# Kernel tuning notes

Measured on AMD Instinct MI355X. Metric: run time of the kernel, lower is better.

Reference implementation:

```python
import jax, jax.numpy as jnp
import numpy as np

K = 20  # neighbors

def _edgeconv(x, W, b):
    # x: [B, C, N]; W: [O, 2C]; b: [O]
    xt = jnp.swapaxes(x, 1, 2)                      # [B, N, C]
    # pairwise (negative squared) distance: -|xi|^2 - 2 xi.xj ... wait torch: -xx - inner - xx^T
    inner = -2.0 * jnp.einsum('bic,bjc->bij', xt, xt)   # [B, N, N]
    xx = jnp.sum(xt * xt, axis=-1)                       # [B, N]
    pd = -xx[:, None, :] - inner - xx[:, :, None]        # [B, N, N]
    _, idx = jax.lax.top_k(pd, K)                        # [B, N, K] nearest neighbors
    # gather neighbor features: feat[b,n,k,:] = xt[b, idx[b,n,k], :]
    feat = jnp.take_along_axis(xt[:, None, :, :],        # [B,1,N,C]
                               idx[:, :, :, None], axis=2)  # [B, N, K, C]
    center = xt[:, :, None, :]                           # [B, N, 1, C]
    edge = jnp.concatenate([feat - center,
                            jnp.broadcast_to(center, feat.shape)], axis=-1)  # [B,N,K,2C]
    # 1x1 conv == linear over channel dim, then LeakyReLU(0.2)
    h = jnp.einsum('bnkc,oc->bnko', edge, W) + b         # [B, N, K, O]
    h = jnp.where(h >= 0, h, 0.2 * h)
    out = jnp.max(h, axis=2)                             # [B, N, O] (max over neighbors)
    return jnp.swapaxes(out, 1, 2)                       # [B, O, N]

def setup_inputs() -> dict:
    key = jax.random.key(0)
    k1, k2, k3 = jax.random.split(key, 3)
    B, C, N, O = 8, 64, 4096, 128
    x = jax.random.normal(k1, (B, C, N), dtype=jnp.float32)
    W = jax.random.normal(k2, (O, 2 * C), dtype=jnp.float32) * (1.0 / np.sqrt(2 * C))
    b = jax.random.normal(k3, (O,), dtype=jnp.float32) * 0.01
    return {"x": x, "W": W, "b": b}

def reference(x, W, b):
    return _edgeconv(x, W, b)
```

## Files before the change

### kernel.cpp

```cpp
#include <hip/hip_runtime.h>

#define BB 8
#define CC 64
#define OO 128
#define NN 4096
#define KNN 20
#define NT 256
#define NG 64
#define NCH 4
#define RING 9
#define TRIG 5
#define SPLITW 192
#define WSPL 384
#define TILEB (16 * SPLITW * 2)

typedef short bf16x8 __attribute__((ext_vector_type(8)));
typedef float f32x4 __attribute__((ext_vector_type(4)));
typedef const __attribute__((address_space(1))) unsigned int* gas_ptr;
typedef __attribute__((address_space(3))) unsigned int* las_ptr;

#define REP20(F, P) F(P,0) F(P,1) F(P,2) F(P,3) F(P,4) F(P,5) F(P,6) F(P,7) \
    F(P,8) F(P,9) F(P,10) F(P,11) F(P,12) F(P,13) F(P,14) F(P,15) F(P,16)   \
    F(P,17) F(P,18) F(P,19)

#define TS_DECL(P,k) float P##m##k = 1e30f; int P##p##k = -1;
#define TS_REPL(P,k)                                                        \
  { const bool _h = (P##kpos == (k));                                       \
    P##m##k = _h ? _d : P##m##k;                                            \
    P##p##k = _h ? _j : P##p##k; }

#define TS_N(vd, xd, va, xa, vb, xb)                                        \
  { const bool _g = (vb) > (va); vd = _g ? (vb) : (va); xd = _g ? (xb) : (xa); }

#define TS_TREE(P)                                                          \
  { float t0,t1,t2,t3,t4,t5,t6,t7,t8,t9; int y0,y1,y2,y3,y4,y5,y6,y7,y8,y9; \
    TS_N(t0,y0, P##m0,0,  P##m1,1)   TS_N(t1,y1, P##m2,2,  P##m3,3)         \
    TS_N(t2,y2, P##m4,4,  P##m5,5)   TS_N(t3,y3, P##m6,6,  P##m7,7)         \
    TS_N(t4,y4, P##m8,8,  P##m9,9)   TS_N(t5,y5, P##m10,10, P##m11,11)      \
    TS_N(t6,y6, P##m12,12, P##m13,13) TS_N(t7,y7, P##m14,14, P##m15,15)     \
    TS_N(t8,y8, P##m16,16, P##m17,17) TS_N(t9,y9, P##m18,18, P##m19,19)     \
    float u0,u1,u2,u3,u4; int z0,z1,z2,z3,z4;                               \
    TS_N(u0,z0, t0,y0, t1,y1) TS_N(u1,z1, t2,y2, t3,y3)                     \
    TS_N(u2,z2, t4,y4, t5,y5) TS_N(u3,z3, t6,y6, t7,y7)                     \
    TS_N(u4,z4, t8,y8, t9,y9)                                               \
    float w0,w1; int q0,q1;                                                 \
    TS_N(w0,q0, u0,z0, u1,z1) TS_N(w1,q1, u2,z2, u3,z3)                     \
    float e0; int r0;                                                       \
    TS_N(e0,r0, w0,q0, w1,q1)                                               \
    TS_N(P##kmax, P##kpos, e0,r0, u4,z4) }

#define TS_INS(P, dval, jval)                                               \
  { const float _d = (dval); const int _j = (jval);                         \
    REP20(TS_REPL, P)                                                       \
    TS_TREE(P) }

#define RT_UPDATE                                                           \
  { const int _s1 = __builtin_amdgcn_ds_swizzle(__float_as_int(A_kmax), 0x101F); \
    const float _m1 = fminf(A_kmax, __int_as_float(_s1));                   \
    const int _s2 = __builtin_amdgcn_ds_swizzle(__float_as_int(_m1), 0x201F); \
    rt = fminf(_m1, __int_as_float(_s2)); }

__device__ __forceinline__ unsigned rne_bf16(float f) {
  const unsigned u = __float_as_uint(f);
  return (u + 0x7fffu + ((u >> 16) & 1u)) >> 16;
}

__global__ __launch_bounds__(128) void wsplit_kernel(
    const float* __restrict__ W, unsigned short* __restrict__ Wsp) {
  const int o = blockIdx.x;
  const int t = threadIdx.x;
  const float w = W[(size_t)o * (2 * CC) + t];
  const unsigned h = rne_bf16(w);
  const float r = w - __uint_as_float(h << 16);
  const unsigned m = rne_bf16(r);
  const float s = r - __uint_as_float(m << 16);
  const unsigned l = rne_bf16(s);
  unsigned short* row = Wsp + (size_t)o * WSPL;
  row[t] = (unsigned short)h;
  row[128 + t] = (unsigned short)m;
  row[256 + t] = (unsigned short)l;
}

__global__ __launch_bounds__(128, 3) void xprep_kernel(
    const float* __restrict__ x, float* __restrict__ xsq,
    unsigned short* __restrict__ xsp) {
  const int b = blockIdx.y;
  const int n = blockIdx.x * 128 + threadIdx.x;
  const float* xb = x + (size_t)b * CC * NN;

  float xr[CC];
  float sq = 0.f;
#pragma unroll
  for (int c = 0; c < CC; ++c) {
    xr[c] = xb[(size_t)c * NN + n];
    sq = fmaf(xr[c], xr[c], sq);
  }
  xsq[(size_t)b * NN + n] = sq;

  unsigned* srow = (unsigned*)(xsp + ((size_t)b * NN + n) * SPLITW);
#pragma unroll
  for (int c = 0; c < CC; c += 2) {
    const unsigned h0 = rne_bf16(xr[c]), h1 = rne_bf16(xr[c + 1]);
    const float r0 = xr[c] - __uint_as_float(h0 << 16);
    const float r1 = xr[c + 1] - __uint_as_float(h1 << 16);
    const unsigned m0 = rne_bf16(r0), m1 = rne_bf16(r1);
    const float s0 = r0 - __uint_as_float(m0 << 16);
    const float s1 = r1 - __uint_as_float(m1 << 16);
    const unsigned l0 = rne_bf16(s0), l1 = rne_bf16(s1);
    srow[c / 2] = h0 | (h1 << 16);
    srow[32 + c / 2] = m0 | (m1 << 16);
    srow[64 + c / 2] = l0 | (l1 << 16);
  }
}

#define MFMA6(ACC, B0, B1, B2, B3, B4, B5)                                  \
  f32x4 ACC;                                                                \
  { f32x4 a0 = {0.f,0.f,0.f,0.f}; f32x4 a1 = {0.f,0.f,0.f,0.f};             \
    f32x4 a2 = {0.f,0.f,0.f,0.f}; f32x4 a3 = {0.f,0.f,0.f,0.f};             \
    a0 = __builtin_amdgcn_mfma_f32_16x16x32_bf16(Ah0, B0, a0, 0, 0, 0);     \
    a1 = __builtin_amdgcn_mfma_f32_16x16x32_bf16(Ah1, B1, a1, 0, 0, 0);     \
    a2 = __builtin_amdgcn_mfma_f32_16x16x32_bf16(Ah0, B2, a2, 0, 0, 0);     \
    a3 = __builtin_amdgcn_mfma_f32_16x16x32_bf16(Ah1, B3, a3, 0, 0, 0);     \
    a0 = __builtin_amdgcn_mfma_f32_16x16x32_bf16(Am0, B0, a0, 0, 0, 0);     \
    a1 = __builtin_amdgcn_mfma_f32_16x16x32_bf16(Am1, B1, a1, 0, 0, 0);     \
    a2 = __builtin_amdgcn_mfma_f32_16x16x32_bf16(Ah0, B4, a2, 0, 0, 0);     \
    a3 = __builtin_amdgcn_mfma_f32_16x16x32_bf16(Ah1, B5, a3, 0, 0, 0);     \
    a0 = __builtin_amdgcn_mfma_f32_16x16x32_bf16(Al0, B0, a0, 0, 0, 0);     \
    a1 = __builtin_amdgcn_mfma_f32_16x16x32_bf16(Al1, B1, a1, 0, 0, 0);     \
    a2 = __builtin_amdgcn_mfma_f32_16x16x32_bf16(Am0, B2, a2, 0, 0, 0);     \
    a3 = __builtin_amdgcn_mfma_f32_16x16x32_bf16(Am1, B3, a3, 0, 0, 0);     \
    ACC = (a0 + a1) + (a2 + a3); }

__global__ __launch_bounds__(256, 3) void aq_kernel(
    const unsigned short* __restrict__ xsp,
    const unsigned short* __restrict__ Wsp, const float* __restrict__ bias,
    unsigned short* __restrict__ Ab16, float* __restrict__ Q) {
  const int b = blockIdx.y;
  const int wv = threadIdx.x >> 6;
  const int lane = threadIdx.x & 63;
  const int q = lane >> 4;
  const int c = lane & 15;
  const int nb = blockIdx.x * 64 + wv * 16;

  const unsigned short* arow =
      xsp + ((size_t)b * NN + nb + c) * SPLITW + q * 8;
  const bf16x8 Ah0 = *(const bf16x8*)(arow);
  const bf16x8 Ah1 = *(const bf16x8*)(arow + 32);
  const bf16x8 Am0 = *(const bf16x8*)(arow + 64);
  const bf16x8 Am1 = *(const bf16x8*)(arow + 96);
  const bf16x8 Al0 = *(const bf16x8*)(arow + 128);
  const bf16x8 Al1 = *(const bf16x8*)(arow + 160);

  unsigned short* Ab = Ab16 + (size_t)b * NN * OO;
  float* Qb = Q + (size_t)b * NN * OO;

#pragma unroll 2
  for (int ot = 0; ot < 8; ++ot) {
    const unsigned short* wrow = Wsp + (size_t)(ot * 16 + c) * WSPL + q * 8;
    const bf16x8 Ph0 = *(const bf16x8*)(wrow);
    const bf16x8 Ph1 = *(const bf16x8*)(wrow + 32);
    const bf16x8 Pm0 = *(const bf16x8*)(wrow + 128);
    const bf16x8 Pm1 = *(const bf16x8*)(wrow + 160);
    const bf16x8 Pl0 = *(const bf16x8*)(wrow + 256);
    const bf16x8 Pl1 = *(const bf16x8*)(wrow + 288);
    MFMA6(accP, Ph0, Ph1, Pm0, Pm1, Pl0, Pl1)
    const bf16x8 Gh0 = *(const bf16x8*)(wrow + 64);
    const bf16x8 Gh1 = *(const bf16x8*)(wrow + 96);
    const bf16x8 Gm0 = *(const bf16x8*)(wrow + 192);
    const bf16x8 Gm1 = *(const bf16x8*)(wrow + 224);
    const bf16x8 Gl0 = *(const bf16x8*)(wrow + 320);
    const bf16x8 Gl1 = *(const bf16x8*)(wrow + 352);
    MFMA6(accG, Gh0, Gh1, Gm0, Gm1, Gl0, Gl1)

    const float bv = bias[ot * 16 + c];
#pragma unroll
    for (int i = 0; i < 4; ++i) {
      const size_t row = (size_t)(nb + q * 4 + i);
      const float p = accP[i];
      Ab[row * OO + ot * 16 + c] = (unsigned short)rne_bf16(p);
      Qb[row * OO + ot * 16 + c] = accG[i] - p + bv;
    }
  }
}

#define STAGEG(G, BUF)                                                      \
  { const char* tb = (const char*)xspB + (size_t)(4 * (G) + wv) * TILEB + gof; \
    char* lb = (char*)(BUF) + wv * 6144;                                    \
    __builtin_amdgcn_global_load_lds((gas_ptr)(const void*)(tb), (las_ptr)(void*)(lb), 16, 0, 0); \
    __builtin_amdgcn_global_load_lds((gas_ptr)(const void*)(tb + 64), (las_ptr)(void*)(lb + 1024), 16, 0, 0); \
    __builtin_amdgcn_global_load_lds((gas_ptr)(const void*)(tb + 128), (las_ptr)(void*)(lb + 2048), 16, 0, 0); \
    __builtin_amdgcn_global_load_lds((gas_ptr)(const void*)(tb + 192), (las_ptr)(void*)(lb + 3072), 16, 0, 0); \
    __builtin_amdgcn_global_load_lds((gas_ptr)(const void*)(tb + 256), (las_ptr)(void*)(lb + 4096), 16, 0, 0); \
    __builtin_amdgcn_global_load_lds((gas_ptr)(const void*)(tb + 320), (las_ptr)(void*)(lb + 5120), 16, 0, 0); }

#define TILE_MFMA_L(LBUF, BUF)                                              \
  { const char* bb = (const char*)(LBUF) + c16;                             \
    const bf16x8 Bh0 = *(const bf16x8*)(bb + (q + 0) * 256);                \
    const bf16x8 Bh1 = *(const bf16x8*)(bb + (q + 4) * 256);                \
    const bf16x8 Bm0 = *(const bf16x8*)(bb + (q + 8) * 256);                \
    const bf16x8 Bm1 = *(const bf16x8*)(bb + (q + 12) * 256);               \
    const bf16x8 Bl0 = *(const bf16x8*)(bb + (q + 16) * 256);               \
    const bf16x8 Bl1 = *(const bf16x8*)(bb + (q + 20) * 256);               \
    f32x4 ac0 = {0.f, 0.f, 0.f, 0.f};                                       \
    f32x4 ac1 = {0.f, 0.f, 0.f, 0.f};                                       \
    f32x4 ac2 = {0.f, 0.f, 0.f, 0.f};                                       \
    f32x4 ac3 = {0.f, 0.f, 0.f, 0.f};                                       \
    ac0 = __builtin_amdgcn_mfma_f32_16x16x32_bf16(Ah0, Bh0, ac0, 0, 0, 0);  \
    ac1 = __builtin_amdgcn_mfma_f32_16x16x32_bf16(Ah1, Bh1, ac1, 0, 0, 0);  \
    ac2 = __builtin_amdgcn_mfma_f32_16x16x32_bf16(Ah0, Bm0, ac2, 0, 0, 0);  \
    ac3 = __builtin_amdgcn_mfma_f32_16x16x32_bf16(Ah1, Bm1, ac3, 0, 0, 0);  \
    ac0 = __builtin_amdgcn_mfma_f32_16x16x32_bf16(Am0, Bh0, ac0, 0, 0, 0);  \
    ac1 = __builtin_amdgcn_mfma_f32_16x16x32_bf16(Am1, Bh1, ac1, 0, 0, 0);  \
    ac2 = __builtin_amdgcn_mfma_f32_16x16x32_bf16(Ah0, Bl0, ac2, 0, 0, 0);  \
    ac3 = __builtin_amdgcn_mfma_f32_16x16x32_bf16(Ah1, Bl1, ac3, 0, 0, 0);  \
    ac0 = __builtin_amdgcn_mfma_f32_16x16x32_bf16(Al0, Bh0, ac0, 0, 0, 0);  \
    ac1 = __builtin_amdgcn_mfma_f32_16x16x32_bf16(Al1, Bh1, ac1, 0, 0, 0);  \
    ac2 = __builtin_amdgcn_mfma_f32_16x16x32_bf16(Am0, Bm0, ac2, 0, 0, 0);  \
    ac3 = __builtin_amdgcn_mfma_f32_16x16x32_bf16(Am1, Bm1, ac3, 0, 0, 0);  \
    const f32x4 acc = (ac0 + ac1) + (ac2 + ac3);                            \
    float* bw = &bounce[BUF][wv][0];                                        \
    bw[(q * 4 + 0) * 20 + c] = acc[0];                                      \
    bw[(q * 4 + 1) * 20 + c] = acc[1];                                      \
    bw[(q * 4 + 2) * 20 + c] = acc[2];                                      \
    bw[(q * 4 + 3) * 20 + c] = acc[3]; }

#define TILE_VALS(T, BUF)                                                   \
  const float* br = &bounce[BUF][wv][myrow * 20 + 4 * g];                   \
  const f32x4 dots = *(const f32x4*)br;                                     \
  const float4 xx = *(const float4*)(xsqb + (T) * 16 + 4 * g);              \
  const float d0 = fmaf(-2.f, dots[0], xx.x);                               \
  const float d1 = fmaf(-2.f, dots[1], xx.y);                               \
  const float d2 = fmaf(-2.f, dots[2], xx.z);                               \
  const float d3 = fmaf(-2.f, dots[3], xx.w);                               \
  const int jb = (T) * 16 + 4 * g;

#define TILE_SELF(T, BUF, K0, K1, K2, K3)                                   \
  { TILE_VALS(T, BUF)                                                       \
    A_m##K0 = d0; A_p##K0 = jb;                                             \
    A_m##K1 = d1; A_p##K1 = jb + 1;                                         \
    A_m##K2 = d2; A_p##K2 = jb + 2;                                         \
    A_m##K3 = d3; A_p##K3 = jb + 3; }

#define TILE_SEL(T, BUF)                                                    \
  { TILE_VALS(T, BUF)                                                       \
    if (d0 <= rt) { myring[cnt] = make_float2(d0, __int_as_float(jb)); ++cnt; } \
    if (d1 <= rt) { myring[cnt] = make_float2(d1, __int_as_float(jb + 1)); ++cnt; } \
    if (d2 <= rt) { myring[cnt] = make_float2(d2, __int_as_float(jb + 2)); ++cnt; } \
    if (d3 <= rt) { myring[cnt] = make_float2(d3, __int_as_float(jb + 3)); ++cnt; } \
    if (__ballot(cnt >= TRIG)) {                                            \
      for (int _k = 0; _k < cnt; ++_k) {                                    \
        const float2 e = myring[_k];                                        \
        if (e.x < A_kmax) { TS_INS(A_, e.x, __float_as_int(e.y)) }          \
      }                                                                     \
      cnt = 0;                                                              \
    }                                                                       \
    RT_UPDATE }

__global__ __launch_bounds__(256, 2) void knn_kernel(
    const unsigned short* __restrict__ xsp, const float* __restrict__ xsq,
    float* __restrict__ cd, int* __restrict__ ci) {
  __shared__ unsigned short Bbuf0[4 * TILEB / 2];
  __shared__ unsigned short Bbuf1[4 * TILEB / 2];
  __shared__ float bounce[2][4][16 * 20];
  __shared__ float2 ring[256][RING];

  const int b = blockIdx.y;
  const int wv = threadIdx.x >> 6;
  const int lane = threadIdx.x & 63;
  const int q = lane >> 4;
  const int c = lane & 15;
  const int c16 = c * 16;
  const int gof = c * 384 + q * 16;
  const int ibase = blockIdx.x * 64 + wv * 16;
  const int myrow = q * 4 + (c & 3);
  const int g = c >> 2;
  const int isel = ibase + myrow;

  const unsigned short* xspB = xsp + (size_t)b * NN * SPLITW;
  const float* xsqb = xsq + (size_t)b * NN;

  const unsigned short* arow = xspB + (size_t)(ibase + c) * SPLITW + q * 8;
  const bf16x8 Ah0 = *(const bf16x8*)(arow);
  const bf16x8 Ah1 = *(const bf16x8*)(arow + 32);
  const bf16x8 Am0 = *(const bf16x8*)(arow + 64);
  const bf16x8 Am1 = *(const bf16x8*)(arow + 96);
  const bf16x8 Al0 = *(const bf16x8*)(arow + 128);
  const bf16x8 Al1 = *(const bf16x8*)(arow + 160);

  REP20(TS_DECL, A_)
  float A_kmax = 1e30f; int A_kpos = 0;
  float rt = 1e30f;
  float2* myring = ring[threadIdx.x];
  int cnt = 0;

  STAGEG(0, Bbuf0)
  __syncthreads();
  STAGEG(1, Bbuf1)
  TILE_MFMA_L(Bbuf0 + 0 * 3072, 0)
  TILE_MFMA_L(Bbuf0 + 1 * 3072, 1) TILE_SELF(0, 0, 0, 1, 2, 3)
  TILE_MFMA_L(Bbuf0 + 2 * 3072, 0) TILE_SELF(1, 1, 4, 5, 6, 7)
  TILE_MFMA_L(Bbuf0 + 3 * 3072, 1) TILE_SELF(2, 0, 8, 9, 10, 11)
  __syncthreads();
  STAGEG(2, Bbuf0)
  TILE_MFMA_L(Bbuf1 + 0 * 3072, 0) TILE_SELF(3, 1, 12, 13, 14, 15)
  TILE_MFMA_L(Bbuf1 + 1 * 3072, 1) TILE_SELF(4, 0, 16, 17, 18, 19)
  TS_TREE(A_)
  RT_UPDATE
  TILE_MFMA_L(Bbuf1 + 2 * 3072, 0) TILE_SEL(5, 1)
  TILE_MFMA_L(Bbuf1 + 3 * 3072, 1) TILE_SEL(6, 0)
  __syncthreads();

  for (int G = 2; G < NG - 1; ++G) {
    unsigned short* cur = (G & 1) ? Bbuf1 : Bbuf0;
    unsigned short* nxt = (G & 1) ? Bbuf0 : Bbuf1;
    STAGEG(G + 1, nxt)
    const int t0 = 4 * G;
    TILE_MFMA_L(cur + 0 * 3072, 0) TILE_SEL(t0 - 1, 1)
    TILE_MFMA_L(cur + 1 * 3072, 1) TILE_SEL(t0, 0)
    TILE_MFMA_L(cur + 2 * 3072, 0) TILE_SEL(t0 + 1, 1)
    TILE_MFMA_L(cur + 3 * 3072, 1) TILE_SEL(t0 + 2, 0)
    __syncthreads();
  }

  TILE_MFMA_L(Bbuf1 + 0 * 3072, 0) TILE_SEL(251, 1)
  TILE_MFMA_L(Bbuf1 + 1 * 3072, 1) TILE_SEL(252, 0)
  TILE_MFMA_L(Bbuf1 + 2 * 3072, 0) TILE_SEL(253, 1)
  TILE_MFMA_L(Bbuf1 + 3 * 3072, 1) TILE_SEL(254, 0)
  TILE_SEL(255, 1)

  for (int _k = 0; _k < cnt; ++_k) {
    const float2 e = myring[_k];
    if (e.x < A_kmax) { TS_INS(A_, e.x, __float_as_int(e.y)) }
  }

  const size_t base = ((size_t)(b * NCH + g) * KNN) * NN + isel;
#define TS_ST(P,k) cd[base + (size_t)(k) * NN] = P##m##k; \
                   ci[base + (size_t)(k) * NN] = P##p##k;
  REP20(TS_ST, A_)
#undef TS_ST
}

#define TK_LIST(OP) OP(0) OP(1) OP(2) OP(3) OP(4) OP(5) OP(6) OP(7) OP(8) \
    OP(9) OP(10) OP(11) OP(12) OP(13) OP(14) OP(15) OP(16) OP(17) OP(18) OP(19)
#define TK_DECL(k) float td##k = 1e30f; int ti##k = -1;
#define TK_SW(a, b)                                                        \
  {                                                                        \
    const bool _s = (td##b < td##a) ||                                     \
                    ((td##b == td##a) && (ti##b < ti##a));                 \
    const float _fa = _s ? td##b : td##a;                                  \
    const float _fb = _s ? td##a : td##b;                                  \
    const int _ia = _s ? ti##b : ti##a;                                    \
    const int _ib = _s ? ti##a : ti##b;                                    \
    td##a = _fa; td##b = _fb; ti##a = _ia; ti##b = _ib;                    \
  }
#define TK_BUBBLE                                                          \
  TK_SW(18, 19) TK_SW(17, 18) TK_SW(16, 17) TK_SW(15, 16) TK_SW(14, 15)    \
  TK_SW(13, 14) TK_SW(12, 13) TK_SW(11, 12) TK_SW(10, 11) TK_SW(9, 10)     \
  TK_SW(8, 9) TK_SW(7, 8) TK_SW(6, 7) TK_SW(5, 6) TK_SW(4, 5)              \
  TK_SW(3, 4) TK_SW(2, 3) TK_SW(1, 2) TK_SW(0, 1)

__global__ __launch_bounds__(128, 4) void merge_kernel(
    const float* __restrict__ cd, const int* __restrict__ ci,
    int* __restrict__ idxf) {
  const int b = blockIdx.y;
  const int n = blockIdx.x * 128 + threadIdx.x;

  TK_LIST(TK_DECL)

  for (int ch = 0; ch < NCH; ++ch) {
    const size_t base = ((size_t)(b * NCH + ch) * KNN) * NN + n;
    for (int s = 0; s < KNN; ++s) {
      const float d = cd[base + (size_t)s * NN];
      const int j = ci[base + (size_t)s * NN];
      if ((d < td19) || ((d == td19) && (j < ti19))) {
        td19 = d;
        ti19 = j;
        TK_BUBBLE
      }
    }
  }

#define TK_STI(k) idxf[((size_t)b * KNN + (k)) * NN + n] = ti##k;
  TK_LIST(TK_STI)
#undef TK_STI
}

__global__ __launch_bounds__(256) void gather_kernel(
    const unsigned short* __restrict__ Ab16, const float* __restrict__ Q,
    const int* __restrict__ idxf, float* __restrict__ out) {
  __shared__ int jidx[KNN][32];
  __shared__ float ob[32][OO + 2];

  const int b = blockIdx.y;
  const int n0 = blockIdx.x * 32;
  const int t = threadIdx.x;
  const int p = t & 63;
  const int h = t >> 6;

  for (int e = t; e < KNN * 32; e += 256) {
    const int k = e >> 5, ii = e & 31;
    jidx[k][ii] = idxf[((size_t)b * KNN + k) * NN + n0 + ii];
  }
  __syncthreads();

  const unsigned short* Ab = Ab16 + (size_t)b * NN * OO;
  const float* Qb = Q + (size_t)b * NN * OO;

  for (int ii = h * 8; ii < h * 8 + 8; ++ii) {
    float m0 = -1e30f, m1 = -1e30f;
#pragma unroll
    for (int k = 0; k < KNN; ++k) {
      const unsigned v =
          *(const unsigned*)(Ab + (size_t)jidx[k][ii] * OO + 2 * p);
      m0 = fmaxf(m0, __uint_as_float(v << 16));
      m1 = fmaxf(m1, __uint_as_float(v & 0xFFFF0000u));
    }
    const float2 qv = *(const float2*)(Qb + (size_t)(n0 + ii) * OO + 2 * p);
    const float h0 = m0 + qv.x;
    const float h1 = m1 + qv.y;
    ob[ii][2 * p] = (h0 >= 0.f) ? h0 : 0.2f * h0;
    ob[ii][2 * p + 1] = (h1 >= 0.f) ? h1 : 0.2f * h1;
  }
  __syncthreads();

  float* ou = out + (size_t)b * OO * NN;
  for (int e = t; e < 32 * OO; e += 256) {
    const int ii = e & 31, oo = e >> 5;
    ou[(size_t)oo * NN + n0 + ii] = ob[ii][oo];
  }
}

extern "C" void kernel_launch(void* const* d_in, const int* in_sizes, int n_in,
                              void* d_out, int out_size, void* d_ws,
                              size_t ws_size, hipStream_t stream) {
  (void)in_sizes;
  (void)n_in;
  (void)out_size;
  (void)ws_size;
  const float* x = (const float*)d_in[0];
  const float* W = (const float*)d_in[1];
  const float* bias = (const float*)d_in[2];
  float* out = (float*)d_out;

  char* ws = (char*)d_ws;
  size_t off = 0;
  unsigned short* Ab16 = (unsigned short*)(ws + off);
  off += (size_t)BB * NN * OO * 2;
  float* Q = (float*)(ws + off);
  off += (size_t)BB * NN * OO * 4;
  float* xsq = (float*)(ws + off);
  off += (size_t)BB * NN * 4;
  unsigned short* xsp = (unsigned short*)(ws + off);
  off += (size_t)BB * NN * SPLITW * 2;
  float* cd = (float*)(ws + off);
  off += (size_t)BB * NCH * KNN * NN * 4;
  int* ci = (int*)(ws + off);
  off += (size_t)BB * NCH * KNN * NN * 4;
  int* idxf = (int*)(ws + off);
  off += (size_t)BB * KNN * NN * 4;
  unsigned short* Wsp = (unsigned short*)(ws + off);
  off += (size_t)OO * WSPL * 2;

  wsplit_kernel<<<dim3(OO), 128, 0, stream>>>(W, Wsp);
  xprep_kernel<<<dim3(NN / 128, BB), 128, 0, stream>>>(x, xsq, xsp);
  knn_kernel<<<dim3(NN / 64, BB), 256, 0, stream>>>(xsp, xsq, cd, ci);
  aq_kernel<<<dim3(NN / 64, BB), 256, 0, stream>>>(xsp, Wsp, bias, Ab16, Q);
  merge_kernel<<<dim3(NN / 128, BB), 128, 0, stream>>>(cd, ci, idxf);
  gather_kernel<<<dim3(NN / 32, BB), 256, 0, stream>>>(Ab16, Q, idxf, out);
}
```

Before: 534.0 us.

## Fuse top-k merge into knn kernel via cross-lane shuffles

The separate merge kernel is removed. Each knn thread now merges the four partial top-20 lists held by lanes in different column groups, using wave shuffles at lane offsets 4, 8 and 12 plus an insertion bubble sort, and lanes with g==0 write the final indices. This drops the global write and read of the candidate distance and index buffers and one kernel launch. In exchange the knn kernel's epilogue gets longer and needs more registers, which could lower occupancy or cause spills. Lanes with g!=0 also do redundant merge work whose shuffle sources may read out-of-range lanes, and those results are simply discarded.

```diff
diff --git a/kernel.cpp b/kernel.cpp
--- a/kernel.cpp
+++ b/kernel.cpp
@@ -7,7 +7,6 @@
 #define KNN 20
 #define NT 256
 #define NG 64
-#define NCH 4
 #define RING 9
 #define TRIG 5
 #define SPLITW 192
@@ -59,6 +58,25 @@
     const float _m1 = fminf(A_kmax, __int_as_float(_s1));                   \
     const int _s2 = __builtin_amdgcn_ds_swizzle(__float_as_int(_m1), 0x201F); \
     rt = fminf(_m1, __int_as_float(_s2)); }
+
+#define TK_LIST(OP) OP(0) OP(1) OP(2) OP(3) OP(4) OP(5) OP(6) OP(7) OP(8) \
+    OP(9) OP(10) OP(11) OP(12) OP(13) OP(14) OP(15) OP(16) OP(17) OP(18) OP(19)
+#define TK_DECL(k) float td##k = 1e30f; int ti##k = -1;
+#define TK_SW(a, b)                                                        \
+  {                                                                        \
+    const bool _s = (td##b < td##a) ||                                     \
+                    ((td##b == td##a) && (ti##b < ti##a));                 \
+    const float _fa = _s ? td##b : td##a;                                  \
+    const float _fb = _s ? td##a : td##b;                                  \
+    const int _ia = _s ? ti##b : ti##a;                                    \
+    const int _ib = _s ? ti##a : ti##b;                                    \
+    td##a = _fa; td##b = _fb; ti##a = _ia; ti##b = _ib;                    \
+  }
+#define TK_BUBBLE                                                          \
+  TK_SW(18, 19) TK_SW(17, 18) TK_SW(16, 17) TK_SW(15, 16) TK_SW(14, 15)    \
+  TK_SW(13, 14) TK_SW(12, 13) TK_SW(11, 12) TK_SW(10, 11) TK_SW(9, 10)     \
+  TK_SW(8, 9) TK_SW(7, 8) TK_SW(6, 7) TK_SW(5, 6) TK_SW(4, 5)              \
+  TK_SW(3, 4) TK_SW(2, 3) TK_SW(1, 2) TK_SW(0, 1)
 
 __device__ __forceinline__ unsigned rne_bf16(float f) {
   const unsigned u = __float_as_uint(f);
@@ -258,7 +276,7 @@
 
 __global__ __launch_bounds__(256, 2) void knn_kernel(
     const unsigned short* __restrict__ xsp, const float* __restrict__ xsq,
-    float* __restrict__ cd, int* __restrict__ ci) {
+    int* __restrict__ idxf) {
   __shared__ unsigned short Bbuf0[4 * TILEB / 2];
   __shared__ unsigned short Bbuf1[4 * TILEB / 2];
   __shared__ float bounce[2][4][16 * 20];
@@ -333,56 +351,30 @@
     if (e.x < A_kmax) { TS_INS(A_, e.x, __float_as_int(e.y)) }
   }
 
-  const size_t base = ((size_t)(b * NCH + g) * KNN) * NN + isel;
-#define TS_ST(P,k) cd[base + (size_t)(k) * NN] = P##m##k; \
-                   ci[base + (size_t)(k) * NN] = P##p##k;
-  REP20(TS_ST, A_)
-#undef TS_ST
-}
-
-#define TK_LIST(OP) OP(0) OP(1) OP(2) OP(3) OP(4) OP(5) OP(6) OP(7) OP(8) \
-    OP(9) OP(10) OP(11) OP(12) OP(13) OP(14) OP(15) OP(16) OP(17) OP(18) OP(19)
-#define TK_DECL(k) float td##k = 1e30f; int ti##k = -1;
-#define TK_SW(a, b)                                                        \
-  {                                                                        \
-    const bool _s = (td##b < td##a) ||                                     \
-                    ((td##b == td##a) && (ti##b < ti##a));                 \
-    const float _fa = _s ? td##b : td##a;                                  \
-    const float _fb = _s ? td##a : td##b;                                  \
-    const int _ia = _s ? ti##b : ti##a;                                    \
-    const int _ib = _s ? ti##a : ti##b;                                    \
-    td##a = _fa; td##b = _fb; ti##a = _ia; ti##b = _ib;                    \
-  }
-#define TK_BUBBLE                                                          \
-  TK_SW(18, 19) TK_SW(17, 18) TK_SW(16, 17) TK_SW(15, 16) TK_SW(14, 15)    \
-  TK_SW(13, 14) TK_SW(12, 13) TK_SW(11, 12) TK_SW(10, 11) TK_SW(9, 10)     \
-  TK_SW(8, 9) TK_SW(7, 8) TK_SW(6, 7) TK_SW(5, 6) TK_SW(4, 5)              \
-  TK_SW(3, 4) TK_SW(2, 3) TK_SW(1, 2) TK_SW(0, 1)
-
-__global__ __launch_bounds__(128, 4) void merge_kernel(
-    const float* __restrict__ cd, const int* __restrict__ ci,
-    int* __restrict__ idxf) {
-  const int b = blockIdx.y;
-  const int n = blockIdx.x * 128 + threadIdx.x;
-
   TK_LIST(TK_DECL)
-
-  for (int ch = 0; ch < NCH; ++ch) {
-    const size_t base = ((size_t)(b * NCH + ch) * KNN) * NN + n;
-    for (int s = 0; s < KNN; ++s) {
-      const float d = cd[base + (size_t)s * NN];
-      const int j = ci[base + (size_t)s * NN];
-      if ((d < td19) || ((d == td19) && (j < ti19))) {
-        td19 = d;
-        ti19 = j;
-        TK_BUBBLE
-      }
-    }
-  }
-
-#define TK_STI(k) idxf[((size_t)b * KNN + (k)) * NN + n] = ti##k;
-  TK_LIST(TK_STI)
+#define MG_OWN(k)                                                           \
+  { const float _d = A_m##k; const int _j = A_p##k;                         \
+    if ((_d < td19) || ((_d == td19) && (_j < ti19))) {                     \
+      td19 = _d; ti19 = _j; TK_BUBBLE } }
+  TK_LIST(MG_OWN)
+#define MG_SH(k, O)                                                         \
+  { const float _d = __shfl(A_m##k, lane + (O), 64);                        \
+    const int _j = __shfl(A_p##k, lane + (O), 64);                          \
+    if ((_d < td19) || ((_d == td19) && (_j < ti19))) {                     \
+      td19 = _d; ti19 = _j; TK_BUBBLE } }
+#define MG_S4(k) MG_SH(k, 4)
+#define MG_S8(k) MG_SH(k, 8)
+#define MG_S12(k) MG_SH(k, 12)
+  TK_LIST(MG_S4)
+  TK_LIST(MG_S8)
+  TK_LIST(MG_S12)
+
+  if (g == 0) {
+    const size_t obase = (size_t)b * KNN * NN + isel;
+#define TK_STI(k) idxf[obase + (size_t)(k) * NN] = ti##k;
+    TK_LIST(TK_STI)
 #undef TK_STI
+  }
 }
 
 __global__ __launch_bounds__(256) void gather_kernel(
@@ -452,10 +444,6 @@
   off += (size_t)BB * NN * 4;
   unsigned short* xsp = (unsigned short*)(ws + off);
   off += (size_t)BB * NN * SPLITW * 2;
-  float* cd = (float*)(ws + off);
-  off += (size_t)BB * NCH * KNN * NN * 4;
-  int* ci = (int*)(ws + off);
-  off += (size_t)BB * NCH * KNN * NN * 4;
   int* idxf = (int*)(ws + off);
   off += (size_t)BB * KNN * NN * 4;
   unsigned short* Wsp = (unsigned short*)(ws + off);
@@ -463,8 +451,7 @@
 
   wsplit_kernel<<<dim3(OO), 128, 0, stream>>>(W, Wsp);
   xprep_kernel<<<dim3(NN / 128, BB), 128, 0, stream>>>(x, xsq, xsp);
-  knn_kernel<<<dim3(NN / 64, BB), 256, 0, stream>>>(xsp, xsq, cd, ci);
+  knn_kernel<<<dim3(NN / 64, BB), 256, 0, stream>>>(xsp, xsq, idxf);
   aq_kernel<<<dim3(NN / 64, BB), 256, 0, stream>>>(xsp, Wsp, bias, Ab16, Q);
-  merge_kernel<<<dim3(NN / 128, BB), 128, 0, stream>>>(cd, ci, idxf);
   gather_kernel<<<dim3(NN / 32, BB), 256, 0, stream>>>(Ab16, Q, idxf, out);
 }
```

Measured after the change: 630.0 us. 1.18x slower.
